# Optimization experiments

Hardware: AMD Instinct MI355X
Metric: run time of the kernel (lower is better)

The kernel has to match this reference:

```python
import jax, jax.numpy as jnp
import numpy as np
import math

N, S, C, K, V = 32, 4096, 1, 512, 128
TARGET_SCALE = 0.06  # normalize_scale == embedding_scale when normalize=True


def setup_inputs() -> dict:
    key = jax.random.key(0)
    k1, k2 = jax.random.split(key)
    x0 = jax.random.normal(k1, (N, S, C, V), dtype=jnp.float32)
    emb = jax.random.normal(k2, (C, K, V), dtype=jnp.float32) * TARGET_SCALE
    # after_update(): renormalize each code vector to norm = embedding_scale*sqrt(V)
    tn = TARGET_SCALE * math.sqrt(V)
    emb = emb * (tn / jnp.linalg.norm(emb, axis=2, keepdims=True))
    return {"x0": x0, "embedding0": emb}


def _vq_forward(x0, embedding0):
    tn = TARGET_SCALE * math.sqrt(V)
    # normalize inputs and codebook to the same norm (normalize=True path)
    x = tn * x0 / jnp.linalg.norm(x0, axis=3, keepdims=True)              # (N,S,C,V)
    emb = tn * embedding0 / jnp.linalg.norm(embedding0, axis=2, keepdims=True)  # (C,K,V)

    xf = x.reshape(N * S, C, V)
    x2 = jnp.sum(xf * xf, axis=2)                     # (NS, C)
    e2 = jnp.sum(emb * emb, axis=2)                   # (C, K)
    dots = jnp.einsum('ncv,ckv->nck', xf, emb)        # (NS, C, K)
    d2 = x2[:, :, None] + e2[None, :, :] - 2.0 * dots
    index = jnp.argmin(d2, axis=2)                    # (NS, C) int

    # entropy of code usage: histc over n_classes, normalized by len(index)=NS
    hist = jnp.zeros((K,), jnp.float32).at[index.reshape(-1)].add(1.0)
    prob = hist / float(N * S)
    entropy = -jnp.sum(jnp.where(hist > 0, prob * jnp.log(jnp.where(hist > 0, prob, 1.0)), 0.0))

    # gather selected code vectors per channel
    output = emb[jnp.arange(C)[None, :], index]       # (NS, C, V)
    output = output.reshape(x.shape)                  # (N,S,C,V)

    sg = jax.lax.stop_gradient
    out0 = sg(output - x) + x                                              # straight-through
    out1 = jnp.sum((sg(x) - output) ** 2, axis=3)                          # codebook loss (N,S,C)
    out2 = jnp.sum((x - sg(output)) ** 2, axis=3) + jnp.sum((x - x0) ** 2, axis=3)  # commitment + norm penalty
    return out0, out1, out2, entropy


def reference(x0, embedding0):
    return _vq_forward(x0, embedding0)
```

## Files before the change

### kernel.cpp

```cpp
#include <hip/hip_runtime.h>
#include <math.h>

#define VDIM   128
#define KCODES 512
#define NROWS  (32 * 4096)
#define TILE_ROWS 128
#define STAGE_CODES 128
#define STAGE_GRAN (STAGE_CODES * 16)
#define TN 0.67882250993908565f

typedef __attribute__((ext_vector_type(8))) short bf16x8;
typedef __attribute__((ext_vector_type(4))) float f32x4;

__device__ __forceinline__ unsigned short f2bf(float f) {
    unsigned u = __float_as_uint(f);
    unsigned r = u + 0x7FFFu + ((u >> 16) & 1u);
    return (unsigned short)(r >> 16);
}

__device__ __forceinline__ bf16x8 pack8(float4 a, float4 b) {
    bf16x8 v;
    v[0] = (short)f2bf(a.x); v[1] = (short)f2bf(a.y);
    v[2] = (short)f2bf(a.z); v[3] = (short)f2bf(a.w);
    v[4] = (short)f2bf(b.x); v[5] = (short)f2bf(b.y);
    v[6] = (short)f2bf(b.z); v[7] = (short)f2bf(b.w);
    return v;
}

__global__ void prep_emb(const float* __restrict__ emb0,
                         float* __restrict__ embn,
                         unsigned short* __restrict__ ebf) {
    int k = blockIdx.x;
    int l = threadIdx.x;
    const float* row = emb0 + (size_t)k * VDIM;
    float a = row[l];
    float b = row[l + 64];
    float ss = a * a + b * b;
    #pragma unroll
    for (int off = 32; off; off >>= 1) ss += __shfl_xor(ss, off);
    float nrm = sqrtf(ss);
    float ea = (TN * a) / nrm;
    float eb = (TN * b) / nrm;
    embn[(size_t)k * VDIM + l]      = ea;
    embn[(size_t)k * VDIM + l + 64] = eb;
    ebf[(size_t)k * VDIM + l]      = f2bf(ea);
    ebf[(size_t)k * VDIM + l + 64] = f2bf(eb);
}

__global__ __launch_bounds__(256, 4) void vq_main(
        const float* __restrict__ x0,
        const unsigned short* __restrict__ ebf,
        const float* __restrict__ embn,
        unsigned* __restrict__ hist,
        float* __restrict__ out0,
        float* __restrict__ out1,
        float* __restrict__ out2) {
    __shared__ uint4 sB[STAGE_GRAN];
    __shared__ int   sbesti[TILE_ROWS];
    __shared__ float sdot[TILE_ROWS];
    __shared__ float sn0[TILE_ROWS];

    int t = threadIdx.x;
    int w = t >> 6;
    int l = t & 63;
    int n15 = l & 15;
    int q = l >> 4;

    int rowbase = blockIdx.x * TILE_ROWS + (w << 5);
    bf16x8 afr[2][4];
    float nsq[2];
    #pragma unroll
    for (int s = 0; s < 2; ++s) {
        const float* xrow = x0 + (size_t)(rowbase + (s << 4) + n15) * VDIM + (q << 3);
        float p0 = 0.f, p1 = 0.f;
        #pragma unroll
        for (int kc = 0; kc < 4; ++kc) {
            const float4* xp = (const float4*)(xrow + (kc << 5));
            float4 a = xp[0], b = xp[1];
            p0 = fmaf(a.x, a.x, p0); p1 = fmaf(a.y, a.y, p1);
            p0 = fmaf(a.z, a.z, p0); p1 = fmaf(a.w, a.w, p1);
            p0 = fmaf(b.x, b.x, p0); p1 = fmaf(b.y, b.y, p1);
            p0 = fmaf(b.z, b.z, p0); p1 = fmaf(b.w, b.w, p1);
            afr[s][kc] = pack8(a, b);
        }
        nsq[s] = p0 + p1;
        nsq[s] += __shfl_xor(nsq[s], 16, 64);
        nsq[s] += __shfl_xor(nsq[s], 32, 64);
    }

    float best[2][4];
    int   bidx[2][4];
    #pragma unroll
    for (int s = 0; s < 2; ++s)
        #pragma unroll
        for (int r = 0; r < 4; ++r) { best[s][r] = -3.4e38f; bidx[s][r] = 0; }

    const f32x4 zero4 = {0.f, 0.f, 0.f, 0.f};
    const uint4* ebg = (const uint4*)ebf;

    for (int st = 0; st < 4; ++st) {
        if (st) __syncthreads();

        #pragma unroll
        for (int r = 0; r < 8; ++r) {
            int code = st * STAGE_CODES + (r << 4) + (t & 15);
            int gran = ((t >> 6) << 2) + ((t >> 4) & 3);
            sB[(r << 8) + t] = ebg[(size_t)code * 16 + gran];
        }
        __syncthreads();

        #pragma unroll 2
        for (int cn8 = 0; cn8 < 8; ++cn8) {
            const bf16x8* bls = ((const bf16x8*)sB) + (cn8 << 8) + l;
            bf16x8 b0 = bls[0], b1 = bls[64], b2 = bls[128], b3 = bls[192];
            int nbase = st * STAGE_CODES + (cn8 << 4) + n15;
            #pragma unroll
            for (int s = 0; s < 2; ++s) {
                f32x4 acc = __builtin_amdgcn_mfma_f32_16x16x32_bf16(afr[s][0], b0, zero4, 0, 0, 0);
                acc = __builtin_amdgcn_mfma_f32_16x16x32_bf16(afr[s][1], b1, acc, 0, 0, 0);
                acc = __builtin_amdgcn_mfma_f32_16x16x32_bf16(afr[s][2], b2, acc, 0, 0, 0);
                acc = __builtin_amdgcn_mfma_f32_16x16x32_bf16(afr[s][3], b3, acc, 0, 0, 0);
                #pragma unroll
                for (int r = 0; r < 4; ++r) {
                    float d = acc[r];
                    if (d > best[s][r]) { best[s][r] = d; bidx[s][r] = nbase; }
                }
            }
        }
    }

    #pragma unroll
    for (int m = 1; m <= 8; m <<= 1) {
        #pragma unroll
        for (int s = 0; s < 2; ++s)
            #pragma unroll
            for (int r = 0; r < 4; ++r) {
                float ov = __shfl_xor(best[s][r], m, 64);
                int   oi = __shfl_xor(bidx[s][r], m, 64);
                if (ov > best[s][r] || (ov == best[s][r] && oi < bidx[s][r])) {
                    best[s][r] = ov; bidx[s][r] = oi;
                }
            }
    }

    if (n15 == 0) {
        #pragma unroll
        for (int s = 0; s < 2; ++s)
            #pragma unroll
            for (int r = 0; r < 4; ++r) {
                int lr = (w << 5) + (s << 4) + (q << 2) + r;
                sbesti[lr] = bidx[s][r];
                sdot[lr]   = best[s][r];
            }
    }
    if (q == 0) {
        #pragma unroll
        for (int s = 0; s < 2; ++s) sn0[(w << 5) + (s << 4) + n15] = nsq[s];
    }
    __syncthreads();

    size_t blockrow = (size_t)blockIdx.x * TILE_ROWS;
    #pragma unroll
    for (int pass = 0; pass < 16; ++pass) {
        int lr = (pass << 3) + (t >> 5);
        int v4 = t & 31;
        int bi = sbesti[lr];
        float4 e = ((const float4*)(embn + (size_t)bi * VDIM))[v4];
        ((float4*)(out0 + (blockrow + lr) * (size_t)VDIM))[v4] = e;
    }

    if (t < TILE_ROWS) {
        size_t row = blockrow + t;
        int bi = sbesti[t];
        float dotv = sdot[t];
        float nn = sn0[t];
        float sc = TN / sqrtf(nn);
        float o1 = 2.f * TN * TN - 2.f * sc * dotv;
        out1[row] = o1;
        float sm = sc - 1.f;
        out2[row] = o1 + sm * sm * nn;
        atomicAdd(&hist[bi], 1u);
    }
}

__global__ void entropy_k(const unsigned* __restrict__ hist,
                          float* __restrict__ out) {
    __shared__ float red[8];
    int t = threadIdx.x;
    float h = (float)hist[t];
    float p = h / (float)NROWS;
    float term = (h > 0.f) ? p * logf(p) : 0.f;
    #pragma unroll
    for (int off = 32; off; off >>= 1) term += __shfl_xor(term, off);
    if ((t & 63) == 0) red[t >> 6] = term;
    __syncthreads();
    if (t == 0) {
        float ssum = 0.f;
        #pragma unroll
        for (int i = 0; i < 8; i++) ssum += red[i];
        out[0] = -ssum;
    }
}

extern "C" void kernel_launch(void* const* d_in, const int* in_sizes, int n_in,
                              void* d_out, int out_size, void* d_ws, size_t ws_size,
                              hipStream_t stream) {
    const float* x0   = (const float*)d_in[0];
    const float* emb0 = (const float*)d_in[1];

    float* embn = (float*)d_ws;
    unsigned* hist = (unsigned*)(embn + (size_t)KCODES * VDIM);
    unsigned short* ebf = (unsigned short*)(hist + KCODES);

    float* out  = (float*)d_out;
    float* out0 = out;
    float* out1 = out0 + (size_t)NROWS * VDIM;
    float* out2 = out1 + NROWS;
    float* oent = out2 + NROWS;

    hipMemsetAsync(hist, 0, KCODES * sizeof(unsigned), stream);
    prep_emb<<<KCODES, 64, 0, stream>>>(emb0, embn, ebf);
    vq_main<<<NROWS / TILE_ROWS, 256, 0, stream>>>(x0, ebf, embn, hist,
                                                   out0, out1, out2);
    entropy_k<<<1, KCODES, 0, stream>>>(hist, oent);
}
```

Measured before the change: 167.0 us.

## Pre-swizzle bf16 codebook into MFMA layout and read it from global, not LDS

The prep kernel now writes the bf16 codebook in the exact fragment order the MFMA loop consumes. The main kernel drops its LDS staging and block barriers and loads the B fragments straight from global memory, where the 128 KB codebook should stay cache-resident. Output stores are also switched to nontemporal stores to reduce cache pollution from the large streaming out0 write. The trade-off is that the B fragments are now global/L2 loads on the MFMA critical path instead of LDS reads.

```diff
diff --git a/kernel.cpp b/kernel.cpp
--- a/kernel.cpp
+++ b/kernel.cpp
@@ -5,8 +5,6 @@
 #define KCODES 512
 #define NROWS  (32 * 4096)
 #define TILE_ROWS 128
-#define STAGE_CODES 128
-#define STAGE_GRAN (STAGE_CODES * 16)
 #define TN 0.67882250993908565f
 
 typedef __attribute__((ext_vector_type(8))) short bf16x8;
@@ -18,12 +16,12 @@
     return (unsigned short)(r >> 16);
 }
 
-__device__ __forceinline__ bf16x8 pack8(float4 a, float4 b) {
+__device__ __forceinline__ bf16x8 pack8(f32x4 a, f32x4 b) {
     bf16x8 v;
-    v[0] = (short)f2bf(a.x); v[1] = (short)f2bf(a.y);
-    v[2] = (short)f2bf(a.z); v[3] = (short)f2bf(a.w);
-    v[4] = (short)f2bf(b.x); v[5] = (short)f2bf(b.y);
-    v[6] = (short)f2bf(b.z); v[7] = (short)f2bf(b.w);
+    v[0] = (short)f2bf(a[0]); v[1] = (short)f2bf(a[1]);
+    v[2] = (short)f2bf(a[2]); v[3] = (short)f2bf(a[3]);
+    v[4] = (short)f2bf(b[0]); v[5] = (short)f2bf(b[1]);
+    v[6] = (short)f2bf(b[2]); v[7] = (short)f2bf(b[3]);
     return v;
 }
 
@@ -43,8 +41,11 @@
     float eb = (TN * b) / nrm;
     embn[(size_t)k * VDIM + l]      = ea;
     embn[(size_t)k * VDIM + l + 64] = eb;
-    ebf[(size_t)k * VDIM + l]      = f2bf(ea);
-    ebf[(size_t)k * VDIM + l + 64] = f2bf(eb);
+    size_t base = ((size_t)(k >> 4) << 11) + ((size_t)(k & 15) << 3);
+    int d1 = l;
+    int d2 = l + 64;
+    ebf[base + ((size_t)(d1 >> 3) << 7) + (d1 & 7)] = f2bf(ea);
+    ebf[base + ((size_t)(d2 >> 3) << 7) + (d2 & 7)] = f2bf(eb);
 }
 
 __global__ __launch_bounds__(256, 4) void vq_main(
@@ -55,7 +56,6 @@
         float* __restrict__ out0,
         float* __restrict__ out1,
         float* __restrict__ out2) {
-    __shared__ uint4 sB[STAGE_GRAN];
     __shared__ int   sbesti[TILE_ROWS];
     __shared__ float sdot[TILE_ROWS];
     __shared__ float sn0[TILE_ROWS];
@@ -75,12 +75,12 @@
         float p0 = 0.f, p1 = 0.f;
         #pragma unroll
         for (int kc = 0; kc < 4; ++kc) {
-            const float4* xp = (const float4*)(xrow + (kc << 5));
-            float4 a = xp[0], b = xp[1];
-            p0 = fmaf(a.x, a.x, p0); p1 = fmaf(a.y, a.y, p1);
-            p0 = fmaf(a.z, a.z, p0); p1 = fmaf(a.w, a.w, p1);
-            p0 = fmaf(b.x, b.x, p0); p1 = fmaf(b.y, b.y, p1);
-            p0 = fmaf(b.z, b.z, p0); p1 = fmaf(b.w, b.w, p1);
+            const f32x4* xp = (const f32x4*)(xrow + (kc << 5));
+            f32x4 a = xp[0], b = xp[1];
+            p0 = fmaf(a[0], a[0], p0); p1 = fmaf(a[1], a[1], p1);
+            p0 = fmaf(a[2], a[2], p0); p1 = fmaf(a[3], a[3], p1);
+            p0 = fmaf(b[0], b[0], p0); p1 = fmaf(b[1], b[1], p1);
+            p0 = fmaf(b[2], b[2], p0); p1 = fmaf(b[3], b[3], p1);
             afr[s][kc] = pack8(a, b);
         }
         nsq[s] = p0 + p1;
@@ -96,35 +96,23 @@
         for (int r = 0; r < 4; ++r) { best[s][r] = -3.4e38f; bidx[s][r] = 0; }
 
     const f32x4 zero4 = {0.f, 0.f, 0.f, 0.f};
-    const uint4* ebg = (const uint4*)ebf;
-
-    for (int st = 0; st < 4; ++st) {
-        if (st) __syncthreads();
-
-        #pragma unroll
-        for (int r = 0; r < 8; ++r) {
-            int code = st * STAGE_CODES + (r << 4) + (t & 15);
-            int gran = ((t >> 6) << 2) + ((t >> 4) & 3);
-            sB[(r << 8) + t] = ebg[(size_t)code * 16 + gran];
-        }
-        __syncthreads();
-
-        #pragma unroll 2
-        for (int cn8 = 0; cn8 < 8; ++cn8) {
-            const bf16x8* bls = ((const bf16x8*)sB) + (cn8 << 8) + l;
-            bf16x8 b0 = bls[0], b1 = bls[64], b2 = bls[128], b3 = bls[192];
-            int nbase = st * STAGE_CODES + (cn8 << 4) + n15;
+    const bf16x8* __restrict__ bt = (const bf16x8*)ebf;
+
+    #pragma unroll 2
+    for (int cn = 0; cn < 32; ++cn) {
+        const bf16x8* bp = bt + (cn << 8) + l;
+        bf16x8 b0 = bp[0], b1 = bp[64], b2 = bp[128], b3 = bp[192];
+        int nbase = (cn << 4) + n15;
+        #pragma unroll
+        for (int s = 0; s < 2; ++s) {
+            f32x4 acc = __builtin_amdgcn_mfma_f32_16x16x32_bf16(afr[s][0], b0, zero4, 0, 0, 0);
+            acc = __builtin_amdgcn_mfma_f32_16x16x32_bf16(afr[s][1], b1, acc, 0, 0, 0);
+            acc = __builtin_amdgcn_mfma_f32_16x16x32_bf16(afr[s][2], b2, acc, 0, 0, 0);
+            acc = __builtin_amdgcn_mfma_f32_16x16x32_bf16(afr[s][3], b3, acc, 0, 0, 0);
             #pragma unroll
-            for (int s = 0; s < 2; ++s) {
-                f32x4 acc = __builtin_amdgcn_mfma_f32_16x16x32_bf16(afr[s][0], b0, zero4, 0, 0, 0);
-                acc = __builtin_amdgcn_mfma_f32_16x16x32_bf16(afr[s][1], b1, acc, 0, 0, 0);
-                acc = __builtin_amdgcn_mfma_f32_16x16x32_bf16(afr[s][2], b2, acc, 0, 0, 0);
-                acc = __builtin_amdgcn_mfma_f32_16x16x32_bf16(afr[s][3], b3, acc, 0, 0, 0);
-                #pragma unroll
-                for (int r = 0; r < 4; ++r) {
-                    float d = acc[r];
-                    if (d > best[s][r]) { best[s][r] = d; bidx[s][r] = nbase; }
-                }
+            for (int r = 0; r < 4; ++r) {
+                float d = acc[r];
+                if (d > best[s][r]) { best[s][r] = d; bidx[s][r] = nbase; }
             }
         }
     }
@@ -165,8 +153,8 @@
         int lr = (pass << 3) + (t >> 5);
         int v4 = t & 31;
         int bi = sbesti[lr];
-        float4 e = ((const float4*)(embn + (size_t)bi * VDIM))[v4];
-        ((float4*)(out0 + (blockrow + lr) * (size_t)VDIM))[v4] = e;
+        f32x4 e = *((const f32x4*)(embn + (size_t)bi * VDIM) + v4);
+        __builtin_nontemporal_store(e, (f32x4*)(out0 + (blockrow + lr) * (size_t)VDIM) + v4);
     }
 
     if (t < TILE_ROWS) {
@@ -176,9 +164,9 @@
         float nn = sn0[t];
         float sc = TN / sqrtf(nn);
         float o1 = 2.f * TN * TN - 2.f * sc * dotv;
-        out1[row] = o1;
+        __builtin_nontemporal_store(o1, &out1[row]);
         float sm = sc - 1.f;
-        out2[row] = o1 + sm * sm * nn;
+        __builtin_nontemporal_store(o1 + sm * sm * nn, &out2[row]);
         atomicAdd(&hist[bi], 1u);
     }
 }
```

After: 165.0 us. Within noise of the previous version (-1.2%).
